# Performance work log

Hardware: AMD Instinct MI355X
Metric: run time of the kernel (lower is better)

The kernel has to match this reference:

```python
import jax, jax.numpy as jnp
from jax import lax
import numpy as np

VTH = 0.2
DECAY = 0.25            # LIF membrane decay used by pcdmd slayers.LIFSpike (STBP-style)
DT = 0.001              # norse default integration step
TAU_SYN_INV = 200.0     # norse LSNNParameters defaults
TAU_MEM_INV = 100.0
TAU_ADAPT_INV = 1.0 / 700.0
BETA = 0.0              # module sets beta=0 (no threshold adaptation jumps)
ALPHA = 100.0           # SuperSpike surrogate slope (norse 'super' method)

@jax.custom_vjp
def spike_rect(v):
    # Heaviside forward, rectangular surrogate backward (STBP)
    return (v > 0).astype(v.dtype)

def _sr_fwd(v):
    return spike_rect(v), v

def _sr_bwd(v, g):
    return (g * (jnp.abs(v) < 0.5).astype(g.dtype),)

spike_rect.defvjp(_sr_fwd, _sr_bwd)

@jax.custom_vjp
def spike_super(v):
    # Heaviside forward, SuperSpike surrogate backward (norse 'super')
    return (v > 0).astype(v.dtype)

def _ss_fwd(v):
    return spike_super(v), v

def _ss_bwd(v, g):
    return (g / (ALPHA * jnp.abs(v) + 1.0) ** 2,)

spike_super.defvjp(_ss_fwd, _ss_bwd)

def lif_spike(x):
    # x: [..., T] -> spike train [..., T]
    # u_t = DECAY * u_{t-1} * (1 - o_{t-1}) + x_t ; o_t = H(u_t - VTH)
    xT = jnp.moveaxis(x, -1, 0)  # [T, ...]
    u0 = jnp.zeros(xT.shape[1:], x.dtype)
    def step(carry, xt):
        u, o = carry
        u = DECAY * u * (1.0 - o) + xt
        o = spike_rect(u - VTH)
        return (u, o), o
    _, out = lax.scan(step, (u0, u0), xT)
    return jnp.moveaxis(out, 0, -1)

def lsnn_recurrent(x, w_in, w_rec):
    # x: [T, B, H] input spikes; norse LSNNRecurrent lsnn_step with beta=0, v_th=VTH
    x_in = jnp.einsum('tbh,oh->tbo', x, w_in)  # input current, hoisted out of scan
    B, H = x.shape[1], w_in.shape[0]
    z0 = jnp.zeros((B, H), x.dtype)
    state0 = (z0, z0, z0, jnp.full((B, H), VTH, x.dtype))  # z, v, i, b (b starts at v_th)
    def step(state, xt):
        z, v, i, b = state
        i_jump = i + xt + z @ w_rec.T
        v_dec = v + DT * TAU_MEM_INV * (-v + i_jump)          # v_leak = 0
        i_dec = i_jump - DT * TAU_SYN_INV * i_jump
        b_dec = b + DT * TAU_ADAPT_INV * (VTH - b)
        z_new = spike_super(v_dec - b_dec)
        v_new = (1.0 - z_new) * v_dec                          # v_reset = 0
        b_new = b_dec + z_new * TAU_ADAPT_INV * BETA
        return (z_new, v_new, i_dec, b_new), z_new
    _, out = lax.scan(step, state0, x_in)
    return out  # [T, B, H]

def setup_inputs() -> dict:
    key = jax.random.key(0)
    ks = jax.random.split(key, 7)
    B, T = 64, 8192
    EEG_C, AUD_C, H, OUT = 64, 1, 10, 2
    x = jax.random.normal(ks[0], (B, 1, EEG_C + 2 * AUD_C, T), jnp.float32)
    s_in = 1.0 / float(np.sqrt(EEG_C))
    s_h = 1.0 / float(np.sqrt(H))
    return {
        'x': x,
        'w_front': jax.random.uniform(ks[1], (H, EEG_C), jnp.float32, -s_in, s_in),
        'b_front': jax.random.uniform(ks[2], (H,), jnp.float32, -s_in, s_in),
        'w_in': jax.random.uniform(ks[3], (H, H), jnp.float32, -s_h, s_h),
        'w_rec': jax.random.uniform(ks[4], (H, H), jnp.float32, -s_h, s_h),
        'w_cls': jax.random.uniform(ks[5], (OUT, H), jnp.float32, -s_h, s_h),
        'b_cls': jax.random.uniform(ks[6], (OUT,), jnp.float32, -s_h, s_h),
    }

def reference(x, w_front, b_front, w_in, w_rec, w_cls, b_cls):
    AUD_C = 1
    window_length = x.shape[-1]
    eeg = x[:, 0, AUD_C:-AUD_C, :]                              # [B, 64, T]
    eeg = jnp.einsum('bct,hc->bht', eeg, w_front) + b_front[None, :, None]
    eeg = lif_spike(eeg)                                        # spike_tanh in snn mode
    eeg = jnp.transpose(eeg, (2, 0, 1))                         # [T, B, H]
    z = lsnn_recurrent(eeg, w_in, w_rec)                        # [T, B, H]
    out = jnp.transpose(z, (1, 2, 0))                           # [B, H, T]
    out = jnp.einsum('bht,oh->bot', out, w_cls) + b_cls[None, :, None]
    out = lif_spike(out)                                        # spike_sigmoid in snn mode
    return jnp.sum(out, axis=2) / window_length                 # [B, 2]
```

## Files before the change

### kernel.cpp

```cpp
#include <hip/hip_runtime.h>
#include <cstdint>
#include <cstddef>

#define T_LEN 8192
#define BATCH 64
#define HID   10
#define CH    66
#define EEG   64
#define SM_STRIDE 8384

__global__ void k_front(const float* __restrict__ x, const float* __restrict__ wf_g,
                        const float* __restrict__ bf_g, float* __restrict__ y) {
    __shared__ float wf[EEG][HID];
    __shared__ float bf[HID];
    int tid = threadIdx.x;
    for (int i = tid; i < EEG * HID; i += 256) {
        int h = i / EEG, c = i % EEG;
        wf[c][h] = wf_g[i];
    }
    if (tid < HID) bf[tid] = bf_g[tid];
    __syncthreads();

    int b = blockIdx.y;
    int t4 = (blockIdx.x * 256 + tid) * 4;
    const float* xb = x + ((size_t)b * CH + 1) * T_LEN + t4;
    float acc[4][HID];
#pragma unroll
    for (int j = 0; j < 4; ++j)
#pragma unroll
        for (int h = 0; h < HID; ++h) acc[j][h] = bf[h];
#pragma unroll 4
    for (int c = 0; c < EEG; ++c) {
        float4 xv = *(const float4*)(xb + (size_t)c * T_LEN);
#pragma unroll
        for (int h = 0; h < HID; ++h) {
            float w = wf[c][h];
            acc[0][h] = fmaf(xv.x, w, acc[0][h]);
            acc[1][h] = fmaf(xv.y, w, acc[1][h]);
            acc[2][h] = fmaf(xv.z, w, acc[2][h]);
            acc[3][h] = fmaf(xv.w, w, acc[3][h]);
        }
    }
    float* yo = y + (size_t)b * HID * T_LEN + t4;
#pragma unroll
    for (int h = 0; h < HID; ++h)
        *(float4*)(yo + (size_t)h * T_LEN) =
            make_float4(acc[0][h], acc[1][h], acc[2][h], acc[3][h]);
}

__global__ __launch_bounds__(64) void k_flif(const float* __restrict__ y,
                                             unsigned short* __restrict__ smask) {
    int c    = blockIdx.x >> 4;
    int bq   = blockIdx.x & 15;
    int lane = threadIdx.x;
    int g = lane >> 4, h = lane & 15;
    int b = bq * 4 + g;
    int hh = h < HID ? h : HID - 1;

    if (c == 0) {
        for (int i = lane; i < 4 * 96; i += 64) {
            int j = i / 96, w = i % 96;
            ((unsigned*)(smask + (size_t)(bq * 4 + j) * SM_STRIDE))[w] = 0u;
        }
    }

    int t0 = c * 256;
    int ts = t0 - 32; if (ts < 0) ts = 0;
    int nf = (t0 + 256 - ts) >> 2;
    const float4* yb = (const float4*)(y + ((size_t)b * HID + hh) * T_LEN + ts);

    float4 A = yb[0], B = yb[1];
    float u = 0.f, o = 0.f;
    unsigned short* smb = smask + (size_t)b * SM_STRIDE + 192;
    for (int f = 0; f < nf; ++f) {
        int nx = f + 2; if (nx > nf - 1) nx = nf - 1;
        float4 C = yb[nx];
        float vv[4] = {A.x, A.y, A.z, A.w};
        int tb = ts + f * 4;
#pragma unroll
        for (int k = 0; k < 4; ++k) {
            u = (o > 0.5f) ? vv[k] : fmaf(0.25f, u, vv[k]);
            bool sp = (u > 0.2f);
            o = sp ? 1.0f : 0.0f;
            unsigned long long bal = __ballot(sp);
            int t = tb + k;
            if (t >= t0 && h == 0)
                smb[t] = (unsigned short)((bal >> (g * 16)) & 0x3FFull);
        }
        A = B; B = C;
    }
}

__global__ __launch_bounds__(64) void k_lsnn(
    const unsigned short* __restrict__ smask,
    const float* __restrict__ w_in, const float* __restrict__ w_rec,
    const float* __restrict__ w_cls, const float* __restrict__ b_cls,
    float* __restrict__ out) {
    __shared__ float T[768];
    int lane = threadIdx.x;
    for (int i = lane; i < 768; i += 64) {
        int r2 = i % 12;
        int m  = (i / 12) & 31;
        int hi = i / (12 * 32);
        const float* wrow = (r2 < HID) ? (w_in + r2 * HID) : (w_cls + (r2 - HID) * HID);
        float s = 0.f;
#pragma unroll
        for (int j = 0; j < 5; ++j)
            if (m & (1u << j)) s += wrow[hi * 5 + j];
        T[i] = s;
    }
    __syncthreads();

    int q = lane / 12;
    int r = lane - q * 12;
    if (q > 4) q = 4;
    int shq = q * 12;
    int id = blockIdx.x * 5 + q;
    bool valid = (id < 8192) && (lane < 60);
    if (id > 8191) id = 8191;
    int b = id >> 7, chunk = id & 127;

    float wb[HID];
#pragma unroll
    for (int j = 0; j < HID; ++j)
        wb[j] = (r < HID) ? w_rec[r * HID + j] : 0.f;
    float bcl = (r >= HID) ? b_cls[r - HID] : 0.f;

    const unsigned short* sm = smask + (size_t)b * SM_STRIDE + (size_t)chunk * 64;

    auto xlook = [&](const uint4& mv, float* X) {
        unsigned hw[8] = { mv.x & 0x3FFu, (mv.x >> 16) & 0x3FFu,
                           mv.y & 0x3FFu, (mv.y >> 16) & 0x3FFu,
                           mv.z & 0x3FFu, (mv.z >> 16) & 0x3FFu,
                           mv.w & 0x3FFu, (mv.w >> 16) & 0x3FFu };
#pragma unroll
        for (int u = 0; u < 8; ++u)
            X[u] = T[(hw[u] & 31u) * 12 + r] + T[384 + (hw[u] >> 5) * 12 + r];
    };

    uint4 mnext = *(const uint4*)(sm + 8);
    float Xc[8], Xn[8], Pc[8], Pn[8];
    { uint4 m0 = *(const uint4*)(sm); xlook(m0, Xc); }
#pragma unroll
    for (int u = 0; u < 8; ++u) { Pc[u] = 0.f; Pn[u] = 0.f; }

    float v = 0.f, cur = 0.f;
    unsigned zmask = 0;
    float uc = 0.f, oc = 0.f, accs = 0.f;

    for (int gr = 0; gr < 32; ++gr) {
        int nb = gr + 2; if (nb > 31) nb = 31;
        uint4 mfar = *(const uint4*)(sm + (size_t)nb * 8);
        xlook(mnext, Xn);
        unsigned zs[8];
#pragma unroll
        for (int u = 0; u < 8; ++u) {
            int zm = (int)zmask;
            float a0 = __int_as_float(__builtin_amdgcn_sbfe(zm, 0, 1) & __float_as_int(wb[0]));
            float a1 = __int_as_float(__builtin_amdgcn_sbfe(zm, 1, 1) & __float_as_int(wb[1]));
            float a2 = __int_as_float(__builtin_amdgcn_sbfe(zm, 2, 1) & __float_as_int(wb[2]));
            float a3 = __int_as_float(__builtin_amdgcn_sbfe(zm, 3, 1) & __float_as_int(wb[3]));
            float a4 = __int_as_float(__builtin_amdgcn_sbfe(zm, 4, 1) & __float_as_int(wb[4]));
            float a5 = __int_as_float(__builtin_amdgcn_sbfe(zm, 5, 1) & __float_as_int(wb[5]));
            float a6 = __int_as_float(__builtin_amdgcn_sbfe(zm, 6, 1) & __float_as_int(wb[6]));
            float a7 = __int_as_float(__builtin_amdgcn_sbfe(zm, 7, 1) & __float_as_int(wb[7]));
            float a8 = __int_as_float(__builtin_amdgcn_sbfe(zm, 8, 1) & __float_as_int(wb[8]));
            float a9 = __int_as_float(__builtin_amdgcn_sbfe(zm, 9, 1) & __float_as_int(wb[9]));
            float s0 = a0 + a1, s1 = a2 + a3, s2 = a4 + a5, s3 = a6 + a7, s4 = a8 + a9;
            float rec = ((s0 + s1) + (s2 + s3)) + s4;

            float ij = (cur + Xc[u]) + rec;
            float vd = v + 0.1f * (ij - v);
            cur = ij - 0.2f * ij;
            bool zb = vd > 0.2f;
            unsigned long long bal = __ballot(zb);
            v = zb ? 0.f : vd;
            zmask = (unsigned)(bal >> shq) & 0x3FFu;
            zs[u] = zmask;
        }
        if (gr >= 21) {
#pragma unroll
            for (int u = 0; u < 8; ++u)
                Pn[u] = T[(zs[u] & 31u) * 12 + r] + T[384 + (zs[u] >> 5) * 12 + r];
        }
        if (gr >= 22) {
            bool in = (gr >= 25);
#pragma unroll
            for (int u = 0; u < 8; ++u) {
                float ci = Pc[u] + bcl;
                uc = (oc > 0.5f) ? ci : fmaf(0.25f, uc, ci);
                oc = (uc > 0.2f) ? 1.f : 0.f;
                if (in) accs += oc;
            }
        }
#pragma unroll
        for (int u = 0; u < 8; ++u) { Xc[u] = Xn[u]; Pc[u] = Pn[u]; }
        mnext = mfar;
    }
#pragma unroll
    for (int u = 0; u < 8; ++u) {
        float ci = Pc[u] + bcl;
        uc = (oc > 0.5f) ? ci : fmaf(0.25f, uc, ci);
        oc = (uc > 0.2f) ? 1.f : 0.f;
        accs += oc;
    }
    if (valid && (r == 10 || r == 11))
        atomicAdd(&out[b * 2 + (r - 10)], accs * (1.0f / 8192.0f));
}

extern "C" void kernel_launch(void* const* d_in, const int* in_sizes, int n_in,
                              void* d_out, int out_size, void* d_ws, size_t ws_size,
                              hipStream_t stream) {
    const float* x       = (const float*)d_in[0];
    const float* w_front = (const float*)d_in[1];
    const float* b_front = (const float*)d_in[2];
    const float* w_in    = (const float*)d_in[3];
    const float* w_rec   = (const float*)d_in[4];
    const float* w_cls   = (const float*)d_in[5];
    const float* b_cls   = (const float*)d_in[6];
    float* out = (float*)d_out;

    float* y = (float*)d_ws;
    unsigned short* smask =
        (unsigned short*)((char*)d_ws + (size_t)BATCH * HID * T_LEN * sizeof(float));

    hipMemsetAsync(out, 0, (size_t)out_size * sizeof(float), stream);
    k_front<<<dim3(T_LEN / 1024, BATCH), 256, 0, stream>>>(x, w_front, b_front, y);
    k_flif<<<dim3(512), 64, 0, stream>>>(y, smask);
    k_lsnn<<<dim3(1639), 64, 0, stream>>>(smask, w_in, w_rec, w_cls, b_cls, out);
}
```

Before: 322.4 us.

## Use DPP row OR for spike mask exchange with 16-lane groups in LSNN

The LSNN kernel changes from five 12-lane groups per wave to four 16-lane groups, so each group lines up with a DPP row. The recurrent spike-mask exchange now uses four DPP row-shift OR steps instead of a full-wave ballot plus shift. The lookup table is padded to a stride of 13, and the mask prefetch distance grows from two groups to four. The trade-off is more blocks (2048 instead of 1639) and more idle lanes per wave, in exchange for a shorter latency on the serial per-step critical path.

```diff
diff --git a/kernel.cpp b/kernel.cpp
--- a/kernel.cpp
+++ b/kernel.cpp
@@ -91,40 +91,48 @@
     }
 }
 
+__device__ __forceinline__ unsigned row_or16(unsigned x) {
+    x |= (unsigned)__builtin_amdgcn_update_dpp(0, (int)x, 0x128, 0xF, 0xF, true);
+    x |= (unsigned)__builtin_amdgcn_update_dpp(0, (int)x, 0x124, 0xF, 0xF, true);
+    x |= (unsigned)__builtin_amdgcn_update_dpp(0, (int)x, 0x122, 0xF, 0xF, true);
+    x |= (unsigned)__builtin_amdgcn_update_dpp(0, (int)x, 0x121, 0xF, 0xF, true);
+    return x;
+}
+
 __global__ __launch_bounds__(64) void k_lsnn(
     const unsigned short* __restrict__ smask,
     const float* __restrict__ w_in, const float* __restrict__ w_rec,
     const float* __restrict__ w_cls, const float* __restrict__ b_cls,
     float* __restrict__ out) {
-    __shared__ float T[768];
+    __shared__ float T[832];
     int lane = threadIdx.x;
-    for (int i = lane; i < 768; i += 64) {
-        int r2 = i % 12;
-        int m  = (i / 12) & 31;
-        int hi = i / (12 * 32);
-        const float* wrow = (r2 < HID) ? (w_in + r2 * HID) : (w_cls + (r2 - HID) * HID);
+    for (int i = lane; i < 832; i += 64) {
+        int hi = i / 416;
+        int rem = i - hi * 416;
+        int m = rem / 13, r2 = rem - m * 13;
         float s = 0.f;
-#pragma unroll
-        for (int j = 0; j < 5; ++j)
-            if (m & (1u << j)) s += wrow[hi * 5 + j];
+        if (r2 < 12) {
+            const float* wrow = (r2 < HID) ? (w_in + r2 * HID) : (w_cls + (r2 - HID) * HID);
+#pragma unroll
+            for (int j = 0; j < 5; ++j)
+                if (m & (1u << j)) s += wrow[hi * 5 + j];
+        }
         T[i] = s;
     }
     __syncthreads();
 
-    int q = lane / 12;
-    int r = lane - q * 12;
-    if (q > 4) q = 4;
-    int shq = q * 12;
-    int id = blockIdx.x * 5 + q;
-    bool valid = (id < 8192) && (lane < 60);
-    if (id > 8191) id = 8191;
+    int q = lane >> 4;
+    int r = lane & 15;
+    int rr = r < 12 ? r : 11;
+    unsigned lanebit = (r < HID) ? (1u << r) : 0u;
+    int id = blockIdx.x * 4 + q;
     int b = id >> 7, chunk = id & 127;
 
     float wb[HID];
 #pragma unroll
     for (int j = 0; j < HID; ++j)
         wb[j] = (r < HID) ? w_rec[r * HID + j] : 0.f;
-    float bcl = (r >= HID) ? b_cls[r - HID] : 0.f;
+    float bcl = (r == 10 || r == 11) ? b_cls[r - HID] : 0.f;
 
     const unsigned short* sm = smask + (size_t)b * SM_STRIDE + (size_t)chunk * 64;
 
@@ -135,10 +143,12 @@
                            mv.w & 0x3FFu, (mv.w >> 16) & 0x3FFu };
 #pragma unroll
         for (int u = 0; u < 8; ++u)
-            X[u] = T[(hw[u] & 31u) * 12 + r] + T[384 + (hw[u] >> 5) * 12 + r];
+            X[u] = T[(hw[u] & 31u) * 13 + rr] + T[416 + (hw[u] >> 5) * 13 + rr];
     };
 
-    uint4 mnext = *(const uint4*)(sm + 8);
+    uint4 mB = *(const uint4*)(sm + 8);
+    uint4 mC = *(const uint4*)(sm + 16);
+    uint4 mD = *(const uint4*)(sm + 24);
     float Xc[8], Xn[8], Pc[8], Pn[8];
     { uint4 m0 = *(const uint4*)(sm); xlook(m0, Xc); }
 #pragma unroll
@@ -149,9 +159,9 @@
     float uc = 0.f, oc = 0.f, accs = 0.f;
 
     for (int gr = 0; gr < 32; ++gr) {
-        int nb = gr + 2; if (nb > 31) nb = 31;
-        uint4 mfar = *(const uint4*)(sm + (size_t)nb * 8);
-        xlook(mnext, Xn);
+        int nb = gr + 4; if (nb > 31) nb = 31;
+        uint4 mE = *(const uint4*)(sm + (size_t)nb * 8);
+        xlook(mB, Xn);
         unsigned zs[8];
 #pragma unroll
         for (int u = 0; u < 8; ++u) {
@@ -173,15 +183,15 @@
             float vd = v + 0.1f * (ij - v);
             cur = ij - 0.2f * ij;
             bool zb = vd > 0.2f;
-            unsigned long long bal = __ballot(zb);
+            unsigned bit = zb ? lanebit : 0u;
             v = zb ? 0.f : vd;
-            zmask = (unsigned)(bal >> shq) & 0x3FFu;
+            zmask = row_or16(bit);
             zs[u] = zmask;
         }
         if (gr >= 21) {
 #pragma unroll
             for (int u = 0; u < 8; ++u)
-                Pn[u] = T[(zs[u] & 31u) * 12 + r] + T[384 + (zs[u] >> 5) * 12 + r];
+                Pn[u] = T[(zs[u] & 31u) * 13 + rr] + T[416 + (zs[u] >> 5) * 13 + rr];
         }
         if (gr >= 22) {
             bool in = (gr >= 25);
@@ -195,7 +205,7 @@
         }
 #pragma unroll
         for (int u = 0; u < 8; ++u) { Xc[u] = Xn[u]; Pc[u] = Pn[u]; }
-        mnext = mfar;
+        mB = mC; mC = mD; mD = mE;
     }
 #pragma unroll
     for (int u = 0; u < 8; ++u) {
@@ -204,7 +214,7 @@
         oc = (uc > 0.2f) ? 1.f : 0.f;
         accs += oc;
     }
-    if (valid && (r == 10 || r == 11))
+    if (r == 10 || r == 11)
         atomicAdd(&out[b * 2 + (r - 10)], accs * (1.0f / 8192.0f));
 }
 
@@ -227,5 +237,5 @@
     hipMemsetAsync(out, 0, (size_t)out_size * sizeof(float), stream);
     k_front<<<dim3(T_LEN / 1024, BATCH), 256, 0, stream>>>(x, w_front, b_front, y);
     k_flif<<<dim3(512), 64, 0, stream>>>(y, smask);
-    k_lsnn<<<dim3(1639), 64, 0, stream>>>(smask, w_in, w_rec, w_cls, b_cls, out);
-}
+    k_lsnn<<<dim3(2048), 64, 0, stream>>>(smask, w_in, w_rec, w_cls, b_cls, out);
+}
```

After: 332.0 us. 1.03x slower.
